# Kernel tuning notes

Hardware: AMD Instinct MI355X
Metric: run time of the kernel (lower is better)

The kernel has to match this reference:

```python
import jax, jax.numpy as jnp
import numpy as np

N = 100_000      # nodes
E = 1_600_000    # edges (avg degree 16)
H = 4            # heads
C = 32           # per-head channels
HID = 128        # hidden = H*C
L = 4            # layers
IN, ED, OUT = 8, 6, 256
NEG_SLOPE = 0.2  # LeakyReLU default in GATv2Conv


def setup_inputs() -> dict:
    key = jax.random.key(0)
    ks = jax.random.split(key, 16)
    s = 0.1
    return {
        "x": jax.random.normal(ks[0], (N, IN), dtype=jnp.float32),
        "edge_index": jax.random.randint(ks[1], (2, E), 0, N, dtype=jnp.int32),
        "edge_attr": jax.random.normal(ks[2], (E, ED), dtype=jnp.float32),
        "W_in": jax.random.normal(ks[3], (IN, HID), dtype=jnp.float32) * s,
        "b_in": jnp.zeros((HID,), jnp.float32),
        "W_l": jax.random.normal(ks[4], (L, HID, HID), dtype=jnp.float32) * s,
        "b_l": jnp.zeros((L, HID), jnp.float32),
        "W_r": jax.random.normal(ks[5], (L, HID, HID), dtype=jnp.float32) * s,
        "b_r": jnp.zeros((L, HID), jnp.float32),
        "W_e": jax.random.normal(ks[6], (L, ED, HID), dtype=jnp.float32) * s,
        "att": jax.random.normal(ks[7], (L, H, C), dtype=jnp.float32) * s,
        "bias": jnp.zeros((L, HID), jnp.float32),
        "ln_w": jnp.ones((L, HID), jnp.float32),
        "ln_b": jnp.zeros((L, HID), jnp.float32),
        "W_out": jax.random.normal(ks[8], (HID, OUT), dtype=jnp.float32) * s,
        "b_out": jnp.zeros((OUT,), jnp.float32),
    }


def _elu(x):
    return jnp.where(x > 0, x, jnp.expm1(x))


def _leaky(x):
    return jnp.where(x > 0, x, NEG_SLOPE * x)


def _layernorm(x, w, b):
    mu = jnp.mean(x, axis=-1, keepdims=True)
    var = jnp.var(x, axis=-1, keepdims=True)
    return (x - mu) * jax.lax.rsqrt(var + 1e-5) * w + b


def _forward(x, edge_index, edge_attr, W_in, b_in, W_l, b_l, W_r, b_r,
             W_e, att, bias, ln_w, ln_b, W_out, b_out):
    src, dst = edge_index[0], edge_index[1]
    # add_self_loops with fill_value='mean': self-loop edge_attr = mean of incoming edge_attr
    deg = jax.ops.segment_sum(jnp.ones((E,), x.dtype), dst, num_segments=N)
    loop_attr = jax.ops.segment_sum(edge_attr, dst, num_segments=N) / jnp.maximum(deg, 1.0)[:, None]
    loops = jnp.arange(N, dtype=src.dtype)
    src_a = jnp.concatenate([src, loops])          # [E+N]
    dst_a = jnp.concatenate([dst, loops])          # [E+N]
    eattr_a = jnp.concatenate([edge_attr, loop_attr], axis=0)  # [E+N, ED]

    h = _elu(x @ W_in + b_in)  # [N, HID]
    for i in range(L):
        res = h
        xl = (h @ W_l[i] + b_l[i]).reshape(N, H, C)   # source transform
        xr = (h @ W_r[i] + b_r[i]).reshape(N, H, C)   # target transform
        ea = (eattr_a @ W_e[i]).reshape(-1, H, C)     # edge transform
        m = _leaky(xl[src_a] + xr[dst_a] + ea)        # [E+N, H, C]
        score = jnp.einsum('ehc,hc->eh', m, att[i])   # [E+N, H]
        # segment softmax over incoming edges per target node
        smax = jax.ops.segment_max(score, dst_a, num_segments=N)[dst_a]
        ex = jnp.exp(score - smax)
        denom = jax.ops.segment_sum(ex, dst_a, num_segments=N)[dst_a]
        alpha = ex / denom                             # [E+N, H]
        out = jax.ops.segment_sum(alpha[:, :, None] * xl[src_a], dst_a,
                                  num_segments=N).reshape(N, HID) + bias[i]
        h = _elu(_layernorm(out + res, ln_w[i], ln_b[i]))
        # dropout: identity (eval mode)
    return h @ W_out + b_out  # [N, OUT]


def reference(x, edge_index, edge_attr, W_in, b_in, W_l, b_l, W_r, b_r,
              W_e, att, bias, ln_w, ln_b, W_out, b_out):
    return _forward(x, edge_index, edge_attr, W_in, b_in, W_l, b_l, W_r, b_r,
                    W_e, att, bias, ln_w, ln_b, W_out, b_out)
```

## Files before the change

### kernel.cpp

```cpp
#include <hip/hip_runtime.h>
#include <hip/hip_bf16.h>
#include <hip/hip_fp16.h>

#define N_NODES 100000
#define N_EDGES 1600000
#define HEADS 4
#define CHN 32
#define HID 128
#define LAYERS 4
#define IN_F 8
#define ED_F 6
#define OUT_F 256
#define NEG_SLOPE 0.2f

typedef _Float16 f16x8 __attribute__((ext_vector_type(8)));
typedef _Float16 f16x4 __attribute__((ext_vector_type(4)));
typedef float f32x4 __attribute__((ext_vector_type(4)));

__device__ __forceinline__ float elu_f(float x) {
    return x > 0.f ? x : expm1f(x);
}


__global__ void hist_kernel(const int* __restrict__ dst, int* __restrict__ fill) {
    int e = blockIdx.x * blockDim.x + threadIdx.x;
    if (e < N_EDGES) atomicAdd(&fill[dst[e]], 1);
}

__global__ void scan1_kernel(const int* __restrict__ cnt, int* __restrict__ bsum) {
    __shared__ int sd[256];
    int t = threadIdx.x;
    int base = blockIdx.x * 1024 + t * 4;
    int s = 0;
#pragma unroll
    for (int j = 0; j < 4; ++j) {
        int i = base + j;
        if (i < N_NODES) s += cnt[i];
    }
    sd[t] = s;
    for (int off = 128; off > 0; off >>= 1) {
        __syncthreads();
        if (t < off) sd[t] += sd[t + off];
    }
    if (t == 0) bsum[blockIdx.x] = sd[0];
}

__global__ void scan2_kernel(int* __restrict__ bsum, int* __restrict__ rowptr, int nb) {
    int run = 0;
    for (int b = 0; b < nb; ++b) {
        int v = bsum[b];
        bsum[b] = run;
        run += v;
    }
    rowptr[N_NODES] = run;
}

__global__ void scan3_kernel(const int* __restrict__ cnt, const int* __restrict__ bsum,
                             int* __restrict__ rowptr) {
    __shared__ int sd[256];
    int t = threadIdx.x;
    int base = blockIdx.x * 1024 + t * 4;
    int v[4];
#pragma unroll
    for (int j = 0; j < 4; ++j) {
        int i = base + j;
        v[j] = (i < N_NODES) ? cnt[i] : 0;
    }
    int s = v[0] + v[1] + v[2] + v[3];
    sd[t] = s;
    __syncthreads();
    for (int off = 1; off < 256; off <<= 1) {
        int xv = (t >= off) ? sd[t - off] : 0;
        __syncthreads();
        sd[t] += xv;
        __syncthreads();
    }
    int excl = sd[t] - s + bsum[blockIdx.x];
    int pre = 0;
#pragma unroll
    for (int j = 0; j < 4; ++j) {
        int i = base + j;
        if (i < N_NODES) rowptr[i] = excl + pre;
        pre += v[j];
    }
}

__global__ void fill_kernel(const int* __restrict__ src, const int* __restrict__ dst,
                            const int* __restrict__ rowptr, int* __restrict__ fill,
                            int2* __restrict__ csr) {
    int e = blockIdx.x * blockDim.x + threadIdx.x;
    if (e >= N_EDGES) return;
    int d = dst[e];
    int p = rowptr[d] + atomicAdd(&fill[d], 1);
    csr[p] = make_int2(src[e] * (HID * 2), e * (ED_F * 4));
}

__global__ void lattr_kernel(const int* __restrict__ rowptr, const int2* __restrict__ csr,
                             const float* __restrict__ eattr, float* __restrict__ lattr) {
    int gid = blockIdx.x * blockDim.x + threadIdx.x;
    if (gid >= N_NODES * ED_F) return;
    int n = gid / ED_F;
    int d = gid - n * ED_F;
    int rp0 = rowptr[n], rp1 = rowptr[n + 1];
    float s = 0.f;
    for (int p = rp0; p < rp1; ++p)
        s += *(const float*)((const char*)eattr + (size_t)csr[p].y + d * 4);
    int deg = rp1 - rp0;
    lattr[gid] = s / (float)(deg > 0 ? deg : 1);
}


__global__ void convw_kernel(const float* __restrict__ W_l, const float* __restrict__ W_r,
                             const float* __restrict__ W_out, __half* __restrict__ wbt) {
    int gid = blockIdx.x * blockDim.x + threadIdx.x;
    if (gid >= 5 * 256 * 128) return;
    int b = gid >> 15;
    int idx = gid & 32767;
    int n = idx >> 7, k = idx & 127;
    float val;
    if (b < 4)
        val = (n < HID) ? W_l[b * HID * HID + k * HID + n]
                        : W_r[b * HID * HID + k * HID + (n - HID)];
    else
        val = W_out[k * OUT_F + n];
    int boff = n * 256 + ((k * 2) ^ ((n & 7) << 4));
    *(__half*)((char*)wbt + (size_t)b * 65536 + boff) = __float2half_rn(val);
}


__global__ void in_kernel(const float* __restrict__ x, const float* __restrict__ Wi,
                          const float* __restrict__ bi, float* __restrict__ h0) {
    int gid = blockIdx.x * blockDim.x + threadIdx.x;
    if (gid >= N_NODES * HID) return;
    int n = gid >> 7, j = gid & 127;
    float acc = bi[j];
#pragma unroll
    for (int k = 0; k < IN_F; ++k) acc = fmaf(x[n * IN_F + k], Wi[k * HID + j], acc);
    h0[gid] = elu_f(acc);
}


#define LDS_B_OFF 16384

template <int MODE>
__global__ __launch_bounds__(256, 2) void gemm_kernel(
    const float* __restrict__ A, const __half* __restrict__ Bt,
    const float* __restrict__ bias0, const float* __restrict__ bias1,
    __half* __restrict__ xl16, float* __restrict__ xr_out, float* __restrict__ outp) {
    __shared__ __align__(16) unsigned char smem[81920];
    int t = threadIdx.x;
    int row0 = blockIdx.x * 64;

#pragma unroll
    for (int it = 0; it < 8; ++it) {
        int idx = it * 256 + t;
        int r = idx >> 5;
        int k4 = (idx & 31) << 2;
        float4 hv = *(const float4*)(A + (size_t)(row0 + r) * HID + k4);
        f16x4 p;
        p[0] = (_Float16)hv.x; p[1] = (_Float16)hv.y;
        p[2] = (_Float16)hv.z; p[3] = (_Float16)hv.w;
        *(f16x4*)(smem + r * 256 + ((k4 * 2) ^ ((r & 7) << 4))) = p;
    }
#pragma unroll
    for (int it = 0; it < 16; ++it) {
        int off = (it * 256 + t) * 16;
        *(float4*)(smem + LDS_B_OFF + off) = *(const float4*)((const char*)Bt + off);
    }
    __syncthreads();

    int wave = t >> 6;
    int lane = t & 63;
    int lc = lane & 15, lr = lane >> 4;
    int cbase = wave * 64;

    f32x4 acc[4][4];
#pragma unroll
    for (int i = 0; i < 4; ++i)
#pragma unroll
        for (int j = 0; j < 4; ++j) acc[i][j] = (f32x4){0.f, 0.f, 0.f, 0.f};

#pragma unroll
    for (int kk = 0; kk < 4; ++kk) {
        int kb = kk * 64 + lr * 16;
        f16x8 av[4], bv[4];
#pragma unroll
        for (int rt = 0; rt < 4; ++rt) {
            int r = rt * 16 + lc;
            av[rt] = *(const f16x8*)(smem + r * 256 + (kb ^ ((r & 7) << 4)));
        }
#pragma unroll
        for (int ct = 0; ct < 4; ++ct) {
            int c = cbase + ct * 16 + lc;
            bv[ct] = *(const f16x8*)(smem + LDS_B_OFF + c * 256 + (kb ^ ((c & 7) << 4)));
        }
#pragma unroll
        for (int rt = 0; rt < 4; ++rt)
#pragma unroll
            for (int ct = 0; ct < 4; ++ct)
                acc[rt][ct] = __builtin_amdgcn_mfma_f32_16x16x32_f16(av[rt], bv[ct],
                                                                     acc[rt][ct], 0, 0, 0);
    }

#pragma unroll
    for (int ct = 0; ct < 4; ++ct) {
        int col = cbase + ct * 16 + lc;
        float bv;
        if (MODE == 0) bv = (col < HID) ? bias0[col] : bias1[col - HID];
        else bv = bias0[col];
#pragma unroll
        for (int rt = 0; rt < 4; ++rt) {
#pragma unroll
            for (int q = 0; q < 4; ++q) {
                int node = row0 + rt * 16 + lr * 4 + q;
                if (node < N_NODES) {
                    float val = acc[rt][ct][q] + bv;
                    if (MODE == 0) {
                        if (col < HID)
                            xl16[(size_t)node * HID + col] = __float2half_rn(val);
                        else
                            xr_out[(size_t)node * HID + (col - HID)] = val;
                    } else {
                        outp[(size_t)node * OUT_F + col] = val;
                    }
                }
            }
        }
    }
}


struct Slot {
    float2 e0, e1, e2;
    __half2 x;
};

__device__ __forceinline__ void slot_issue(Slot& s, const int2* __restrict__ csr, int& pi,
                                           const char* eab, const char* xlb) {
    int2 se = csr[pi]; ++pi;
    const char* eb = eab + (size_t)se.y;
    s.e0 = *(const float2*)eb;
    s.e1 = *(const float2*)(eb + 8);
    s.e2 = *(const float2*)(eb + 16);
    s.x = *(const __half2*)(xlb + (size_t)se.x);
}

__device__ __forceinline__ void slot_consume(const Slot& sl, const float* we0, const float* we1,
                                             float at0, float at1, float xr0, float xr1,
                                             float& denom, float& acc0, float& acc1) {
    float2 xv = __half22float2(sl.x);
    float ea0 = sl.e0.x * we0[0]; ea0 = fmaf(sl.e0.y, we0[1], ea0);
    ea0 = fmaf(sl.e1.x, we0[2], ea0); ea0 = fmaf(sl.e1.y, we0[3], ea0);
    ea0 = fmaf(sl.e2.x, we0[4], ea0); ea0 = fmaf(sl.e2.y, we0[5], ea0);
    float ea1 = sl.e0.x * we1[0]; ea1 = fmaf(sl.e0.y, we1[1], ea1);
    ea1 = fmaf(sl.e1.x, we1[2], ea1); ea1 = fmaf(sl.e1.y, we1[3], ea1);
    ea1 = fmaf(sl.e2.x, we1[4], ea1); ea1 = fmaf(sl.e2.y, we1[5], ea1);
    float m0 = xv.x + xr0 + ea0;
    float m1 = xv.y + xr1 + ea1;
    m0 = m0 > 0.f ? m0 : NEG_SLOPE * m0;
    m1 = m1 > 0.f ? m1 : NEG_SLOPE * m1;
    float t = fmaf(m1, at1, m0 * at0);
    t += __shfl_xor(t, 1);
    t += __shfl_xor(t, 2);
    t += __shfl_xor(t, 4);
    t += __shfl_xor(t, 8);
    float ex = __expf(t);
    denom += ex;
    acc0 = fmaf(ex, xv.x, acc0);
    acc1 = fmaf(ex, xv.y, acc1);
}

__global__ __launch_bounds__(64, 8) void edge_kernel(
    const __half* __restrict__ xl, const float* __restrict__ xr,
    const float* __restrict__ hcur, float* __restrict__ hnext,
    const int* __restrict__ rowptr, const int2* __restrict__ csr,
    const float* __restrict__ eattr, const float* __restrict__ lattr,
    const float* __restrict__ We, const float* __restrict__ att,
    const float* __restrict__ bias_l, const float* __restrict__ lnw,
    const float* __restrict__ lnb) {
    int v = blockIdx.x;
    int lane = threadIdx.x;
    int c0 = lane * 2;

    float we0[ED_F], we1[ED_F];
#pragma unroll
    for (int d = 0; d < ED_F; ++d) {
        float2 w = *(const float2*)(We + d * HID + c0);
        we0[d] = w.x; we1[d] = w.y;
    }
    float2 atv = *(const float2*)(att + c0);
    float at0 = atv.x, at1 = atv.y;
    float2 xrv = *(const float2*)(xr + (size_t)v * HID + c0);
    float xr0 = xrv.x, xr1 = xrv.y;
    int rp0 = rowptr[v], rp1 = rowptr[v + 1];

    const char* xlb = (const char*)xl + (size_t)c0 * 2;
    const char* eab = (const char*)eattr;

    float denom, acc0, acc1;
    {
        const float2* la = (const float2*)(lattr + (size_t)v * ED_F);
        Slot sl;
        sl.e0 = la[0]; sl.e1 = la[1]; sl.e2 = la[2];
        sl.x = *(const __half2*)(xlb + (size_t)v * (HID * 2));
        denom = 0.f; acc0 = 0.f; acc1 = 0.f;
        slot_consume(sl, we0, we1, at0, at1, xr0, xr1, denom, acc0, acc1);
    }

    int num = rp1 - rp0;
    int pi = rp0;

    Slot sA, sB;
    if (num > 0) slot_issue(sA, csr, pi, eab, xlb);
    if (num > 1) slot_issue(sB, csr, pi, eab, xlb);
    int j = 0;
    for (; j + 2 <= num; j += 2) {
        slot_consume(sA, we0, we1, at0, at1, xr0, xr1, denom, acc0, acc1);
        if (pi < rp1) slot_issue(sA, csr, pi, eab, xlb);
        slot_consume(sB, we0, we1, at0, at1, xr0, xr1, denom, acc0, acc1);
        if (pi < rp1) slot_issue(sB, csr, pi, eab, xlb);
    }
    if (j < num)
        slot_consume(sA, we0, we1, at0, at1, xr0, xr1, denom, acc0, acc1);

    float rd = 1.f / denom;
    acc0 *= rd;
    acc1 *= rd;

    float2 resv = *(const float2*)(hcur + (size_t)v * HID + c0);
    float2 bv = *(const float2*)(bias_l + c0);
    float y0 = acc0 + bv.x + resv.x;
    float y1 = acc1 + bv.y + resv.y;
    float s = y0 + y1;
    float sq = y0 * y0 + y1 * y1;
#pragma unroll
    for (int off = 1; off < 64; off <<= 1) {
        s += __shfl_xor(s, off);
        sq += __shfl_xor(sq, off);
    }
    float mu = s * (1.f / HID);
    float var = sq * (1.f / HID) - mu * mu;
    float rstd = rsqrtf(var + 1e-5f);
    float2 wv = *(const float2*)(lnw + c0);
    float2 lb = *(const float2*)(lnb + c0);
    float n0 = (y0 - mu) * rstd * wv.x + lb.x;
    float n1 = (y1 - mu) * rstd * wv.y + lb.y;
    float2 o;
    o.x = elu_f(n0);
    o.y = elu_f(n1);
    *(float2*)(hnext + (size_t)v * HID + c0) = o;
}


extern "C" void kernel_launch(void* const* d_in, const int* in_sizes, int n_in,
                              void* d_out, int out_size, void* d_ws, size_t ws_size,
                              hipStream_t stream) {
    const float* x     = (const float*)d_in[0];
    const int*   ei    = (const int*)d_in[1];
    const float* eattr = (const float*)d_in[2];
    const float* W_in  = (const float*)d_in[3];
    const float* b_in  = (const float*)d_in[4];
    const float* W_l   = (const float*)d_in[5];
    const float* b_l   = (const float*)d_in[6];
    const float* W_r   = (const float*)d_in[7];
    const float* b_r   = (const float*)d_in[8];
    const float* W_e   = (const float*)d_in[9];
    const float* att   = (const float*)d_in[10];
    const float* bias  = (const float*)d_in[11];
    const float* lnw   = (const float*)d_in[12];
    const float* lnb   = (const float*)d_in[13];
    const float* W_out = (const float*)d_in[14];
    const float* b_out = (const float*)d_in[15];
    float* out = (float*)d_out;

    float* h0    = (float*)d_ws;
    float* h1    = h0 + (size_t)N_NODES * HID;
    float* lattr = h1 + (size_t)N_NODES * HID;
    int* rowptr  = (int*)(lattr + (size_t)N_NODES * ED_F);
    int* fill    = rowptr + (N_NODES + 1);
    int2* csr    = (int2*)(fill + N_NODES);
    int* bsum    = (int*)(csr + N_EDGES);
    __half* wbt  = (__half*)(bsum + 128);

    float*  xr = out;
    __half* xl = (__half*)(out + (size_t)N_NODES * HID);

    const int* srcv = ei;
    const int* dstv = ei + N_EDGES;

    hipMemsetAsync(fill, 0, N_NODES * sizeof(int), stream);
    hist_kernel<<<(N_EDGES + 255) / 256, 256, 0, stream>>>(dstv, fill);
    int nb = (N_NODES + 1023) / 1024;
    scan1_kernel<<<nb, 256, 0, stream>>>(fill, bsum);
    scan2_kernel<<<1, 1, 0, stream>>>(bsum, rowptr, nb);
    scan3_kernel<<<nb, 256, 0, stream>>>(fill, bsum, rowptr);
    hipMemsetAsync(fill, 0, N_NODES * sizeof(int), stream);
    fill_kernel<<<(N_EDGES + 255) / 256, 256, 0, stream>>>(srcv, dstv, rowptr, fill, csr);
    lattr_kernel<<<(N_NODES * ED_F + 255) / 256, 256, 0, stream>>>(rowptr, csr, eattr, lattr);

    convw_kernel<<<(5 * 256 * 128 + 255) / 256, 256, 0, stream>>>(W_l, W_r, W_out, wbt);
    in_kernel<<<(N_NODES * HID) / 256, 256, 0, stream>>>(x, W_in, b_in, h0);

    int gemm_grid = (N_NODES + 63) / 64;
    float* hc = h0;
    float* hn = h1;
    for (int l = 0; l < LAYERS; ++l) {
        gemm_kernel<0><<<gemm_grid, 256, 0, stream>>>(
            hc, wbt + (size_t)l * 32768, b_l + (size_t)l * HID, b_r + (size_t)l * HID,
            xl, xr, nullptr);
        edge_kernel<<<N_NODES, 64, 0, stream>>>(
            xl, xr, hc, hn, rowptr, csr, eattr, lattr,
            W_e + (size_t)l * ED_F * HID, att + (size_t)l * HEADS * CHN,
            bias + (size_t)l * HID, lnw + (size_t)l * HID, lnb + (size_t)l * HID);
        float* tmp = hc; hc = hn; hn = tmp;
    }

    gemm_kernel<1><<<gemm_grid, 256, 0, stream>>>(
        hc, wbt + (size_t)4 * 32768, b_out, nullptr, nullptr, nullptr, out);
}
```

Baseline: 1.115 ms.

## Process two edges per wave with fp16 padded edge attributes and fdot2

The edge kernel now splits the 64-lane wave into two halves, each handling alternate edges with 4 channels per lane, and merges the partial softmax sums with a cross-half shuffle. Edge attributes are converted once to fp16 and padded to 16 bytes so each edge needs a single 16-byte load, and the edge-feature projection uses packed fp16 dot products. The self-loop is folded into the same slot pipeline. This cuts per-edge instruction count and gather traffic, at the cost of fp16 precision on edge attributes and weights, plus an extra conversion pass.

```diff
diff --git a/kernel.cpp b/kernel.cpp
--- a/kernel.cpp
+++ b/kernel.cpp
@@ -15,10 +15,37 @@
 
 typedef _Float16 f16x8 __attribute__((ext_vector_type(8)));
 typedef _Float16 f16x4 __attribute__((ext_vector_type(4)));
+typedef _Float16 h2 __attribute__((ext_vector_type(2)));
 typedef float f32x4 __attribute__((ext_vector_type(4)));
+
+#if defined(__has_builtin)
+#if __has_builtin(__builtin_amdgcn_fdot2)
+#define HAVE_FDOT2 1
+#endif
+#endif
 
 __device__ __forceinline__ float elu_f(float x) {
     return x > 0.f ? x : expm1f(x);
+}
+
+__device__ __forceinline__ h2 bith2(float f) {
+    union { float f; h2 h; } u; u.f = f; return u.h;
+}
+
+__device__ __forceinline__ float dot6(h2 e01, h2 e23, h2 e45, const h2* w) {
+#ifdef HAVE_FDOT2
+    return __builtin_amdgcn_fdot2(e45, w[2],
+           __builtin_amdgcn_fdot2(e23, w[1],
+           __builtin_amdgcn_fdot2(e01, w[0], 0.f, false), false), false);
+#else
+    float s = (float)e01[0] * (float)w[0][0];
+    s = fmaf((float)e01[1], (float)w[0][1], s);
+    s = fmaf((float)e23[0], (float)w[1][0], s);
+    s = fmaf((float)e23[1], (float)w[1][1], s);
+    s = fmaf((float)e45[0], (float)w[2][0], s);
+    s = fmaf((float)e45[1], (float)w[2][1], s);
+    return s;
+#endif
 }
 
 
@@ -92,21 +119,34 @@
     if (e >= N_EDGES) return;
     int d = dst[e];
     int p = rowptr[d] + atomicAdd(&fill[d], 1);
-    csr[p] = make_int2(src[e] * (HID * 2), e * (ED_F * 4));
+    csr[p] = make_int2(src[e] * (HID * 2), e * 16);
+}
+
+__global__ void ecvt_kernel(const float* __restrict__ eattr, __half* __restrict__ ea16) {
+    int gid = blockIdx.x * blockDim.x + threadIdx.x;
+    if (gid >= N_EDGES * 8) return;
+    int e = gid >> 3, d = gid & 7;
+    float v = (d < ED_F) ? eattr[e * ED_F + d] : 0.f;
+    ea16[gid] = __float2half_rn(v);
 }
 
 __global__ void lattr_kernel(const int* __restrict__ rowptr, const int2* __restrict__ csr,
-                             const float* __restrict__ eattr, float* __restrict__ lattr) {
+                             const float* __restrict__ eattr, __half* __restrict__ lat16) {
     int gid = blockIdx.x * blockDim.x + threadIdx.x;
-    if (gid >= N_NODES * ED_F) return;
-    int n = gid / ED_F;
-    int d = gid - n * ED_F;
-    int rp0 = rowptr[n], rp1 = rowptr[n + 1];
+    if (gid >= N_NODES * 8) return;
+    int n = gid >> 3;
+    int d = gid & 7;
     float s = 0.f;
-    for (int p = rp0; p < rp1; ++p)
-        s += *(const float*)((const char*)eattr + (size_t)csr[p].y + d * 4);
-    int deg = rp1 - rp0;
-    lattr[gid] = s / (float)(deg > 0 ? deg : 1);
+    if (d < ED_F) {
+        int rp0 = rowptr[n], rp1 = rowptr[n + 1];
+        for (int p = rp0; p < rp1; ++p) {
+            int eid = csr[p].y >> 4;
+            s += eattr[(size_t)eid * ED_F + d];
+        }
+        int deg = rp1 - rp0;
+        s /= (float)(deg > 0 ? deg : 1);
+    }
+    lat16[gid] = __float2half_rn(s);
 }
 
 
@@ -231,124 +271,142 @@
 
 
 struct Slot {
-    float2 e0, e1, e2;
-    __half2 x;
+    float4 er;
+    float2 xv;
 };
 
-__device__ __forceinline__ void slot_issue(Slot& s, const int2* __restrict__ csr, int& pi,
-                                           const char* eab, const char* xlb) {
-    int2 se = csr[pi]; ++pi;
-    const char* eb = eab + (size_t)se.y;
-    s.e0 = *(const float2*)eb;
-    s.e1 = *(const float2*)(eb + 8);
-    s.e2 = *(const float2*)(eb + 16);
-    s.x = *(const __half2*)(xlb + (size_t)se.x);
-}
-
-__device__ __forceinline__ void slot_consume(const Slot& sl, const float* we0, const float* we1,
-                                             float at0, float at1, float xr0, float xr1,
-                                             float& denom, float& acc0, float& acc1) {
-    float2 xv = __half22float2(sl.x);
-    float ea0 = sl.e0.x * we0[0]; ea0 = fmaf(sl.e0.y, we0[1], ea0);
-    ea0 = fmaf(sl.e1.x, we0[2], ea0); ea0 = fmaf(sl.e1.y, we0[3], ea0);
-    ea0 = fmaf(sl.e2.x, we0[4], ea0); ea0 = fmaf(sl.e2.y, we0[5], ea0);
-    float ea1 = sl.e0.x * we1[0]; ea1 = fmaf(sl.e0.y, we1[1], ea1);
-    ea1 = fmaf(sl.e1.x, we1[2], ea1); ea1 = fmaf(sl.e1.y, we1[3], ea1);
-    ea1 = fmaf(sl.e2.x, we1[4], ea1); ea1 = fmaf(sl.e2.y, we1[5], ea1);
-    float m0 = xv.x + xr0 + ea0;
-    float m1 = xv.y + xr1 + ea1;
-    m0 = m0 > 0.f ? m0 : NEG_SLOPE * m0;
-    m1 = m1 > 0.f ? m1 : NEG_SLOPE * m1;
-    float t = fmaf(m1, at1, m0 * at0);
+__device__ __forceinline__ void slot_issue(Slot& s, int i, int total, int rp0,
+                                           const int2* __restrict__ csr,
+                                           const char* eab, const char* lat16v,
+                                           const char* xlb, int vbytes) {
+    i = min(i, total - 1);
+    const char* eb;
+    const char* xb;
+    if (i == 0) {
+        eb = lat16v;
+        xb = xlb + (size_t)vbytes;
+    } else {
+        int2 se = csr[rp0 + i - 1];
+        eb = eab + (size_t)se.y;
+        xb = xlb + (size_t)se.x;
+    }
+    s.er = *(const float4*)eb;
+    s.xv = *(const float2*)xb;
+}
+
+__device__ __forceinline__ void slot_consume(const Slot& sl, int i, int total,
+                                             const h2 we_h2[4][3], const float* attv,
+                                             const float* xrv,
+                                             float& denom, float* acc) {
+    h2 e01 = bith2(sl.er.x), e23 = bith2(sl.er.y), e45 = bith2(sl.er.z);
+    h2 x01 = bith2(sl.xv.x), x23 = bith2(sl.xv.y);
+    float xf[4];
+    xf[0] = (float)x01[0]; xf[1] = (float)x01[1];
+    xf[2] = (float)x23[0]; xf[3] = (float)x23[1];
+    float t = 0.f;
+#pragma unroll
+    for (int c = 0; c < 4; ++c) {
+        float ea = dot6(e01, e23, e45, we_h2[c]);
+        float m = xf[c] + xrv[c] + ea;
+        m = m > 0.f ? m : NEG_SLOPE * m;
+        t = fmaf(m, attv[c], t);
+    }
     t += __shfl_xor(t, 1);
     t += __shfl_xor(t, 2);
     t += __shfl_xor(t, 4);
-    t += __shfl_xor(t, 8);
     float ex = __expf(t);
+    ex = (i < total) ? ex : 0.f;
     denom += ex;
-    acc0 = fmaf(ex, xv.x, acc0);
-    acc1 = fmaf(ex, xv.y, acc1);
+#pragma unroll
+    for (int c = 0; c < 4; ++c) acc[c] = fmaf(ex, xf[c], acc[c]);
 }
 
 __global__ __launch_bounds__(64, 8) void edge_kernel(
     const __half* __restrict__ xl, const float* __restrict__ xr,
     const float* __restrict__ hcur, float* __restrict__ hnext,
     const int* __restrict__ rowptr, const int2* __restrict__ csr,
-    const float* __restrict__ eattr, const float* __restrict__ lattr,
+    const __half* __restrict__ ea16, const __half* __restrict__ lat16,
     const float* __restrict__ We, const float* __restrict__ att,
     const float* __restrict__ bias_l, const float* __restrict__ lnw,
     const float* __restrict__ lnb) {
     int v = blockIdx.x;
     int lane = threadIdx.x;
-    int c0 = lane * 2;
-
-    float we0[ED_F], we1[ED_F];
-#pragma unroll
-    for (int d = 0; d < ED_F; ++d) {
-        float2 w = *(const float2*)(We + d * HID + c0);
-        we0[d] = w.x; we1[d] = w.y;
-    }
-    float2 atv = *(const float2*)(att + c0);
-    float at0 = atv.x, at1 = atv.y;
-    float2 xrv = *(const float2*)(xr + (size_t)v * HID + c0);
-    float xr0 = xrv.x, xr1 = xrv.y;
+    int half = lane >> 5;
+    int hl = lane & 31;
+    int c0 = hl * 4;
+
+    h2 we_h2[4][3];
+#pragma unroll
+    for (int c = 0; c < 4; ++c)
+#pragma unroll
+        for (int d = 0; d < 3; ++d) {
+            h2 w;
+            w[0] = (_Float16)We[(2 * d) * HID + c0 + c];
+            w[1] = (_Float16)We[(2 * d + 1) * HID + c0 + c];
+            we_h2[c][d] = w;
+        }
+    float4 at4 = *(const float4*)(att + c0);
+    float attv[4] = {at4.x, at4.y, at4.z, at4.w};
+    float4 xr4 = *(const float4*)(xr + (size_t)v * HID + c0);
+    float xrv[4] = {xr4.x, xr4.y, xr4.z, xr4.w};
+
     int rp0 = rowptr[v], rp1 = rowptr[v + 1];
+    int total = (rp1 - rp0) + 1;
+    int R = (total + 1) >> 1;
 
     const char* xlb = (const char*)xl + (size_t)c0 * 2;
-    const char* eab = (const char*)eattr;
-
-    float denom, acc0, acc1;
-    {
-        const float2* la = (const float2*)(lattr + (size_t)v * ED_F);
-        Slot sl;
-        sl.e0 = la[0]; sl.e1 = la[1]; sl.e2 = la[2];
-        sl.x = *(const __half2*)(xlb + (size_t)v * (HID * 2));
-        denom = 0.f; acc0 = 0.f; acc1 = 0.f;
-        slot_consume(sl, we0, we1, at0, at1, xr0, xr1, denom, acc0, acc1);
-    }
-
-    int num = rp1 - rp0;
-    int pi = rp0;
+    const char* eab = (const char*)ea16;
+    const char* lat16v = (const char*)lat16 + (size_t)v * 16;
+    int vbytes = v * (HID * 2);
+
+    float denom = 0.f;
+    float acc[4] = {0.f, 0.f, 0.f, 0.f};
 
     Slot sA, sB;
-    if (num > 0) slot_issue(sA, csr, pi, eab, xlb);
-    if (num > 1) slot_issue(sB, csr, pi, eab, xlb);
-    int j = 0;
-    for (; j + 2 <= num; j += 2) {
-        slot_consume(sA, we0, we1, at0, at1, xr0, xr1, denom, acc0, acc1);
-        if (pi < rp1) slot_issue(sA, csr, pi, eab, xlb);
-        slot_consume(sB, we0, we1, at0, at1, xr0, xr1, denom, acc0, acc1);
-        if (pi < rp1) slot_issue(sB, csr, pi, eab, xlb);
-    }
-    if (j < num)
-        slot_consume(sA, we0, we1, at0, at1, xr0, xr1, denom, acc0, acc1);
+    slot_issue(sA, half, total, rp0, csr, eab, lat16v, xlb, vbytes);
+    if (R > 1) slot_issue(sB, 2 + half, total, rp0, csr, eab, lat16v, xlb, vbytes);
+    int r = 0;
+    for (; r + 2 <= R; r += 2) {
+        slot_consume(sA, 2 * r + half, total, we_h2, attv, xrv, denom, acc);
+        if (r + 2 < R) slot_issue(sA, 2 * (r + 2) + half, total, rp0, csr, eab, lat16v, xlb, vbytes);
+        slot_consume(sB, 2 * (r + 1) + half, total, we_h2, attv, xrv, denom, acc);
+        if (r + 3 < R) slot_issue(sB, 2 * (r + 3) + half, total, rp0, csr, eab, lat16v, xlb, vbytes);
+    }
+    if (r < R) slot_consume(sA, 2 * r + half, total, we_h2, attv, xrv, denom, acc);
+
+    denom += __shfl_xor(denom, 32);
+#pragma unroll
+    for (int c = 0; c < 4; ++c) acc[c] += __shfl_xor(acc[c], 32);
 
     float rd = 1.f / denom;
-    acc0 *= rd;
-    acc1 *= rd;
-
-    float2 resv = *(const float2*)(hcur + (size_t)v * HID + c0);
-    float2 bv = *(const float2*)(bias_l + c0);
-    float y0 = acc0 + bv.x + resv.x;
-    float y1 = acc1 + bv.y + resv.y;
-    float s = y0 + y1;
-    float sq = y0 * y0 + y1 * y1;
-#pragma unroll
-    for (int off = 1; off < 64; off <<= 1) {
+
+    float4 res4 = *(const float4*)(hcur + (size_t)v * HID + c0);
+    float4 bv4 = *(const float4*)(bias_l + c0);
+    float y[4];
+    y[0] = acc[0] * rd + bv4.x + res4.x;
+    y[1] = acc[1] * rd + bv4.y + res4.y;
+    y[2] = acc[2] * rd + bv4.z + res4.z;
+    y[3] = acc[3] * rd + bv4.w + res4.w;
+    float s = y[0] + y[1] + y[2] + y[3];
+    float sq = fmaf(y[0], y[0], fmaf(y[1], y[1], fmaf(y[2], y[2], y[3] * y[3])));
+#pragma unroll
+    for (int off = 1; off < 32; off <<= 1) {
         s += __shfl_xor(s, off);
         sq += __shfl_xor(sq, off);
     }
     float mu = s * (1.f / HID);
     float var = sq * (1.f / HID) - mu * mu;
     float rstd = rsqrtf(var + 1e-5f);
-    float2 wv = *(const float2*)(lnw + c0);
-    float2 lb = *(const float2*)(lnb + c0);
-    float n0 = (y0 - mu) * rstd * wv.x + lb.x;
-    float n1 = (y1 - mu) * rstd * wv.y + lb.y;
-    float2 o;
-    o.x = elu_f(n0);
-    o.y = elu_f(n1);
-    *(float2*)(hnext + (size_t)v * HID + c0) = o;
+    float4 wv4 = *(const float4*)(lnw + c0);
+    float4 lb4 = *(const float4*)(lnb + c0);
+    if (half == 0) {
+        float4 o;
+        o.x = elu_f((y[0] - mu) * rstd * wv4.x + lb4.x);
+        o.y = elu_f((y[1] - mu) * rstd * wv4.y + lb4.y);
+        o.z = elu_f((y[2] - mu) * rstd * wv4.z + lb4.z);
+        o.w = elu_f((y[3] - mu) * rstd * wv4.w + lb4.w);
+        *(float4*)(hnext + (size_t)v * HID + c0) = o;
+    }
 }
 
 
@@ -375,15 +433,16 @@
 
     float* h0    = (float*)d_ws;
     float* h1    = h0 + (size_t)N_NODES * HID;
-    float* lattr = h1 + (size_t)N_NODES * HID;
-    int* rowptr  = (int*)(lattr + (size_t)N_NODES * ED_F);
+    __half* lat16 = (__half*)(h1 + (size_t)N_NODES * HID);
+    int* rowptr  = (int*)(lat16 + (size_t)N_NODES * 8);
     int* fill    = rowptr + (N_NODES + 1);
     int2* csr    = (int2*)(fill + N_NODES);
     int* bsum    = (int*)(csr + N_EDGES);
     __half* wbt  = (__half*)(bsum + 128);
 
-    float*  xr = out;
-    __half* xl = (__half*)(out + (size_t)N_NODES * HID);
+    float*  xr   = out;
+    __half* xl   = (__half*)(out + (size_t)N_NODES * HID);
+    __half* ea16 = xl + (size_t)N_NODES * HID;
 
     const int* srcv = ei;
     const int* dstv = ei + N_EDGES;
@@ -396,7 +455,8 @@
     scan3_kernel<<<nb, 256, 0, stream>>>(fill, bsum, rowptr);
     hipMemsetAsync(fill, 0, N_NODES * sizeof(int), stream);
     fill_kernel<<<(N_EDGES + 255) / 256, 256, 0, stream>>>(srcv, dstv, rowptr, fill, csr);
-    lattr_kernel<<<(N_NODES * ED_F + 255) / 256, 256, 0, stream>>>(rowptr, csr, eattr, lattr);
+    ecvt_kernel<<<(N_EDGES * 8 + 255) / 256, 256, 0, stream>>>(eattr, ea16);
+    lattr_kernel<<<(N_NODES * 8 + 255) / 256, 256, 0, stream>>>(rowptr, csr, eattr, lat16);
 
     convw_kernel<<<(5 * 256 * 128 + 255) / 256, 256, 0, stream>>>(W_l, W_r, W_out, wbt);
     in_kernel<<<(N_NODES * HID) / 256, 256, 0, stream>>>(x, W_in, b_in, h0);
@@ -409,7 +469,7 @@
             hc, wbt + (size_t)l * 32768, b_l + (size_t)l * HID, b_r + (size_t)l * HID,
             xl, xr, nullptr);
         edge_kernel<<<N_NODES, 64, 0, stream>>>(
-            xl, xr, hc, hn, rowptr, csr, eattr, lattr,
+            xl, xr, hc, hn, rowptr, csr, ea16, lat16,
             W_e + (size_t)l * ED_F * HID, att + (size_t)l * HEADS * CHN,
             bias + (size_t)l * HID, lnw + (size_t)l * HID, lnb + (size_t)l * HID);
         float* tmp = hc; hc = hn; hn = tmp;
```

Result: faster. 1.084 ms (-2.7%).
